# Kernel optimization log

Hardware: AMD Instinct MI355X
Metric: run time of the kernel (lower is better)

The kernel has to match this reference:

```python
import jax, jax.numpy as jnp
import numpy as np

B, T, D, H = 4, 2048, 1024, 16
DH = D // H  # 64

def setup_inputs() -> dict:
    key = jax.random.key(0)
    ks = jax.random.split(key, 5)
    scale = 1.0 / np.sqrt(DH)
    return {
        "x": jax.random.normal(ks[0], (B, T, D), dtype=jnp.float32),
        "Wq": jax.random.normal(ks[1], (H, DH, DH), dtype=jnp.float32) * scale,
        "Wk": jax.random.normal(ks[2], (H, DH, DH), dtype=jnp.float32) * scale,
        "Wv": jax.random.normal(ks[3], (H, DH, DH), dtype=jnp.float32) * scale,
        "Wout": jax.random.normal(ks[4], (D, D), dtype=jnp.float32) * (1.0 / np.sqrt(D)),
    }

def reference(x, Wq, Wk, Wv, Wout):
    b, t, d = x.shape
    xh = x.reshape(b, t, H, DH)  # split into heads (b, t, h, dh)
    # torch Linear: y = x @ W.T -> contract input dim with last dim of W
    Q = jnp.einsum('bthd,hed->bthe', xh, Wq)
    K = jnp.einsum('bthd,hed->bthe', xh, Wk)
    V = jnp.einsum('bthd,hed->bthe', xh, Wv)
    scale = 1.0 / jnp.sqrt(jnp.asarray(DH, dtype=x.dtype))
    scores = jnp.einsum('bqhd,bkhd->bhqk', Q, K) * scale  # (b, h, T, T)
    weights = jax.nn.softmax(scores, axis=-1)
    attn = jnp.einsum('bhqk,bkhd->bqhd', weights, V)  # (b, T, h, dh)
    attn = attn.reshape(b, t, d)  # concat heads
    return attn @ Wout.T
```

## Files before the change

### kernel.cpp

```cpp
#include <hip/hip_runtime.h>
#include <hip/hip_bf16.h>

#define BB 4
#define TT 2048
#define DD 1024
#define HH 16

typedef __bf16 bf16;
typedef __bf16 bf16x8 __attribute__((ext_vector_type(8)));
typedef __bf16 bf16x4 __attribute__((ext_vector_type(4)));
typedef float f32x4 __attribute__((ext_vector_type(4)));
typedef float f32x16 __attribute__((ext_vector_type(16)));
typedef unsigned int u32;
typedef u32 u32x4 __attribute__((ext_vector_type(4)));

#define MFMA16(a, b, c) __builtin_amdgcn_mfma_f32_16x16x32_bf16(a, b, c, 0, 0, 0)
#define MFMA32(a, b, c) __builtin_amdgcn_mfma_f32_32x32x16_bf16(a, b, c, 0, 0, 0)

#define C1 0.18033688011112042f

typedef __attribute__((address_space(1))) const u32 gau32;
typedef __attribute__((address_space(3))) u32 lau32;
static __device__ __forceinline__ void gload_lds16(const void* g, void* l) {
    __builtin_amdgcn_global_load_lds((gau32*)g, (lau32*)l, 16, 0, 0);
}

static __device__ __forceinline__ u32 cvtpk(float a, float b) {
    u32 r;
    asm("v_cvt_pk_bf16_f32 %0, %1, %2" : "=v"(r) : "v"(a), "v"(b));
    return r;
}

static __device__ __forceinline__ float rexp2(float x) {
#if __has_builtin(__builtin_amdgcn_exp2f)
    return __builtin_amdgcn_exp2f(x);
#else
    float r;
    asm("v_exp_f32 %0, %1" : "=v"(r) : "v"(x));
    return r;
#endif
}

__global__ __launch_bounds__(256) void k_cvtall(const float* __restrict__ wo, const float* __restrict__ wq,
                                                const float* __restrict__ wk, const float* __restrict__ wv,
                                                bf16* __restrict__ ob, bf16* __restrict__ qb,
                                                bf16* __restrict__ kb, bf16* __restrict__ vb) {
    int i = (blockIdx.x * 256 + threadIdx.x) * 4;
    const float* s;
    bf16* d;
    int off;
    if (i < DD * DD) {
        s = wo; d = ob; off = i;
    } else {
        int j = i - DD * DD;
        int wsel = j >> 16;
        off = j & 65535;
        s = wsel == 0 ? wq : (wsel == 1 ? wk : wv);
        d = wsel == 0 ? qb : (wsel == 1 ? kb : vb);
    }
    f32x4 v = *reinterpret_cast<const f32x4*>(s + off);
    bf16x4 r;
    r[0] = (bf16)v[0]; r[1] = (bf16)v[1]; r[2] = (bf16)v[2]; r[3] = (bf16)v[3];
    *reinterpret_cast<bf16x4*>(d + off) = r;
}

__global__ __launch_bounds__(256) void k_qkv(const float* __restrict__ x,
                                             const bf16* __restrict__ Wq,
                                             const bf16* __restrict__ Wk,
                                             const bf16* __restrict__ Wv,
                                             bf16* __restrict__ Qb,
                                             bf16* __restrict__ Kb,
                                             bf16* __restrict__ VT) {
    __shared__ float xs[4][32 * 64];
    const int w = threadIdx.x >> 6, lane = threadIdx.x & 63;
    const int c = lane & 15, g = lane >> 4;
    const int bh = blockIdx.y;
    const int b = bh >> 4, h = bh & 15;
    const int tb = blockIdx.x * 128 + w * 32;

    float* xw = xs[w];
    {
        const int lr = lane >> 4;
        const int lch = lane & 15;
#pragma unroll
        for (int p = 0; p < 8; p++) {
            const int r = p * 4 + lr;
            const int ch = lch ^ (r & 15);
            gload_lds16(x + ((size_t)(b * TT + tb + r)) * DD + h * 64 + ch * 4,
                        (char*)xw + p * 1024);
        }
    }
    asm volatile("s_waitcnt vmcnt(0)" ::: "memory");

    bf16x8 a[2][2];
#pragma unroll
    for (int s = 0; s < 2; s++)
#pragma unroll
        for (int dt = 0; dt < 2; dt++) {
            const int r = 16 * s + c;
            const int c0 = 8 * dt + 2 * g;
            f32x4 lo = *reinterpret_cast<const f32x4*>(&xw[r * 64 + (c0 ^ (r & 15)) * 4]);
            f32x4 hi = *reinterpret_cast<const f32x4*>(&xw[r * 64 + ((c0 + 1) ^ (r & 15)) * 4]);
            u32x4 u;
            u[0] = cvtpk(lo[0], lo[1]);
            u[1] = cvtpk(lo[2], lo[3]);
            u[2] = cvtpk(hi[0], hi[1]);
            u[3] = cvtpk(hi[2], hi[3]);
            a[s][dt] = __builtin_bit_cast(bf16x8, u);
        }

    const bf16* const Ws[3] = {Wq, Wk, Wv};
    f32x4 acc[3][2][4];
#pragma unroll
    for (int m = 0; m < 3; m++)
#pragma unroll
        for (int s = 0; s < 2; s++)
#pragma unroll
            for (int e = 0; e < 4; e++)
#pragma unroll
                for (int r = 0; r < 4; r++) acc[m][s][e][r] = 0.0f;

#pragma unroll
    for (int m = 0; m < 3; m++) {
#pragma unroll
        for (int eg = 0; eg < 4; eg++) {
#pragma unroll
            for (int dt = 0; dt < 2; dt++) {
                bf16x8 bf = *reinterpret_cast<const bf16x8*>(
                    Ws[m] + (size_t)(h * 64 + 16 * eg + c) * 64 + 32 * dt + 8 * g);
#pragma unroll
                for (int s = 0; s < 2; s++)
                    acc[m][s][eg] = MFMA16(a[s][dt], bf, acc[m][s][eg]);
            }
        }
    }

    bf16* const outs[2] = {Qb, Kb};
#pragma unroll
    for (int m = 0; m < 2; m++)
#pragma unroll
        for (int s = 0; s < 2; s++)
#pragma unroll
            for (int eg = 0; eg < 4; eg++)
#pragma unroll
                for (int r = 0; r < 4; r++) {
                    int t = tb + 16 * s + 4 * g + r;
                    float sv = acc[m][s][eg][r];
                    if (m == 0) sv *= C1;
                    outs[m][((size_t)bh * TT + t) * 64 + 16 * eg + c] = (bf16)sv;
                }

    bf16* vl = (bf16*)xs[w];
#pragma unroll
    for (int s = 0; s < 2; s++)
#pragma unroll
        for (int eg = 0; eg < 4; eg++) {
            bf16x4 v4;
#pragma unroll
            for (int r = 0; r < 4; r++) v4[r] = (bf16)acc[2][s][eg][r];
            *reinterpret_cast<bf16x4*>(&vl[(16 * eg + c) * 40 + 16 * s + 4 * g]) = v4;
        }
#pragma unroll
    for (int n = 0; n < 8; n++) {
        const int np = (n & 4) | ((n & 1) << 1) | ((n >> 1) & 1);
        bf16x4 v = *reinterpret_cast<bf16x4*>(&vl[lane * 40 + 4 * n]);
        *reinterpret_cast<bf16x4*>(&VT[((size_t)bh * 64 + lane) * TT + tb + 4 * np]) = v;
    }
}

#define ATTN_TILE(SKC, SVC, SKN, SVN, T)                                                        \
    do {                                                                                        \
        if ((T) < 31) {                                                                         \
            gload_lds16(kgsrc0 + (size_t)((T) + 1) * 4096, &(SKN)[w * 512]);                    \
            gload_lds16(kgsrc1 + (size_t)((T) + 1) * 4096, &(SKN)[2048 + w * 512]);             \
            gload_lds16(vgsrc0 + (size_t)((T) + 1) * 64, &(SVN)[w * 512]);                      \
            gload_lds16(vgsrc1 + (size_t)((T) + 1) * 64, &(SVN)[2048 + w * 512]);               \
        }                                                                                       \
        f32x16 s0, s1;                                                                          \
        _Pragma("unroll") for (int i = 0; i < 16; i++) { s0[i] = 0.0f; s1[i] = 0.0f; }          \
        __builtin_amdgcn_s_setprio(1);                                                          \
        _Pragma("unroll") for (int d = 0; d < 4; d++) {                                         \
            bf16x8 ka0 = *reinterpret_cast<const bf16x8*>(&(SKC)[roff + d * 1024 + goff0]);     \
            bf16x8 ka1 = *reinterpret_cast<const bf16x8*>(&(SKC)[roff + d * 1024 + goff1]);     \
            s0 = MFMA32(ka0, aq[d], s0);                                                        \
            s1 = MFMA32(ka1, aq[d], s1);                                                        \
        }                                                                                       \
        __builtin_amdgcn_s_setprio(0);                                                          \
        u32 pk[2][4][2];                                                                        \
        _Pragma("unroll") for (int r = 0; r < 16; r++) { float p = rexp2(s0[r]); psum += p; s0[r] = p; } \
        _Pragma("unroll") for (int r = 0; r < 16; r++) { float p = rexp2(s1[r]); psum += p; s1[r] = p; } \
        _Pragma("unroll") for (int m = 0; m < 4; m++)                                           \
            _Pragma("unroll") for (int b2 = 0; b2 < 2; b2++) {                                  \
                pk[0][m][b2] = cvtpk(s0[4 * m + 2 * b2], s0[4 * m + 2 * b2 + 1]);               \
                pk[1][m][b2] = cvtpk(s1[4 * m + 2 * b2], s1[4 * m + 2 * b2 + 1]);               \
            }                                                                                   \
        __builtin_amdgcn_s_setprio(1);                                                          \
        _Pragma("unroll") for (int kt = 0; kt < 4; kt++) {                                      \
            u32x4 pu;                                                                           \
            pu[0] = pk[kt >> 1][2 * (kt & 1)][0];                                               \
            pu[1] = pk[kt >> 1][2 * (kt & 1)][1];                                               \
            pu[2] = pk[kt >> 1][2 * (kt & 1) + 1][0];                                           \
            pu[3] = pk[kt >> 1][2 * (kt & 1) + 1][1];                                           \
            bf16x8 pb = __builtin_bit_cast(bf16x8, pu);                                         \
            bf16x8 va0 = *reinterpret_cast<const bf16x8*>(&(SVC)[roff + kt * 1024 + goff0]);    \
            bf16x8 va1 = *reinterpret_cast<const bf16x8*>(&(SVC)[roff + kt * 1024 + goff1]);    \
            o0 = MFMA32(va0, pb, o0);                                                           \
            o1 = MFMA32(va1, pb, o1);                                                           \
        }                                                                                       \
        __builtin_amdgcn_s_setprio(0);                                                         \
        __syncthreads();                                                                        \
    } while (0)

__global__ __launch_bounds__(256, 4) void k_attn(const bf16* __restrict__ Qb,
                                                 const bf16* __restrict__ Kb,
                                                 const bf16* __restrict__ VT,
                                                 bf16* __restrict__ AO) {
    __shared__ bf16 sK[2][64 * 64];
    __shared__ bf16 sV[2][64 * 64];
    const int w = threadIdx.x >> 6, lane = threadIdx.x & 63;
    const int q = lane & 31, h = lane >> 5;
    const int bid = blockIdx.x;
    const int swz = (bid & 7) * 128 + (bid >> 3);
    const int bh = swz >> 4;
    const int qb = (swz & 15) * 128 + w * 32;
    const bf16* Qh = Qb + (size_t)bh * TT * 64;
    const bf16* Kh = Kb + (size_t)bh * TT * 64;
    const bf16* Vh = VT + (size_t)bh * 64 * TT;

    const int gp = lane & 7;
    int st[2], sj[2];
#pragma unroll
    for (int p = 0; p < 2; p++) {
        const int rp = p * 32 + w * 8 + (lane >> 3);
        const int u_ = rp & 15, J1 = rp >> 4;
        const int e_ = gp ^ (u_ & 7);
        st[p] = 32 * (e_ >> 2) + 16 * (e_ & 1) + u_;
        sj[p] = 2 * J1 + ((e_ >> 1) & 1);
    }
    const bf16* kgsrc0 = Kh + (size_t)st[0] * 64 + sj[0] * 8;
    const bf16* kgsrc1 = Kh + (size_t)st[1] * 64 + sj[1] * 8;
    const bf16* vgsrc0 = Vh + (size_t)st[0] * TT + sj[0] * 8;
    const bf16* vgsrc1 = Vh + (size_t)st[1] * TT + sj[1] * 8;

    gload_lds16(kgsrc0, &sK[0][w * 512]);
    gload_lds16(kgsrc1, &sK[0][2048 + w * 512]);
    gload_lds16(vgsrc0, &sV[0][w * 512]);
    gload_lds16(vgsrc1, &sV[0][2048 + w * 512]);

    bf16x8 aq[4];
#pragma unroll
    for (int d = 0; d < 4; d++)
        aq[d] = *reinterpret_cast<const bf16x8*>(Qh + (size_t)(qb + q) * 64 + 16 * d + 8 * h);

    const int vv = 2 * h + ((q >> 4) & 1);
    const int gl = vv ^ (q & 3);
    const int gb2 = (q >> 2) & 1;
    const int roff = (q & 15) * 64;
    const int goff0 = (4 * gb2 + gl) * 8;
    const int goff1 = (4 * (1 ^ gb2) + gl) * 8;

    f32x16 o0, o1;
#pragma unroll
    for (int i = 0; i < 16; i++) { o0[i] = 0.0f; o1[i] = 0.0f; }
    float psum = 0.0f;

    __syncthreads();

    for (int tp = 0; tp < 16; tp++) {
        ATTN_TILE(sK[0], sV[0], sK[1], sV[1], 2 * tp);
        ATTN_TILE(sK[1], sV[1], sK[0], sV[0], 2 * tp + 1);
    }

    const float l = psum + __shfl_xor(psum, 32);
    const float linv = 1.0f / l;

    const size_t obase = ((size_t)bh * TT + qb + q) * 64;
#pragma unroll
    for (int dg = 0; dg < 2; dg++)
#pragma unroll
        for (int m = 0; m < 4; m++) {
            bf16x4 v;
#pragma unroll
            for (int j = 0; j < 4; j++) {
                const float ov = dg ? o1[4 * m + j] : o0[4 * m + j];
                v[j] = (bf16)(ov * linv);
            }
            *reinterpret_cast<bf16x4*>(AO + obase + 32 * dg + 8 * m + 4 * h) = v;
        }
}

#define OSTAGE(BUF, H)                                                                          \
    do {                                                                                        \
        const bf16* Ab = AO + ((size_t)(b * HH + (H)) * TT + t0) * 64;                          \
        const bf16* Bb = Wo + (size_t)nb * DD + (H) * 64;                                       \
        _Pragma("unroll") for (int p = 0; p < 4; p++) {                                         \
            const int r = p * 32 + w * 8 + (lane >> 3);                                         \
            const int jj = (lane & 7) ^ (r & 7);                                                \
            gload_lds16(Ab + (size_t)r * 64 + jj * 8, &sA[BUF][p * 2048 + w * 512]);            \
            gload_lds16(Bb + (size_t)r * DD + jj * 8, &sB[BUF][p * 2048 + w * 512]);            \
        }                                                                                       \
    } while (0)

__global__ __launch_bounds__(256, 2) void k_oproj(const bf16* __restrict__ AO,
                                                  const bf16* __restrict__ Wo,
                                                  float* __restrict__ out) {
    __shared__ bf16 sA[2][128 * 64];
    __shared__ bf16 sB[2][128 * 64];
    const int w = threadIdx.x >> 6, lane = threadIdx.x & 63;
    const int c = lane & 15, g = lane >> 4;
    const int bid = blockIdx.x;
    const int nb = (bid & 7) * 128;
    const int row0 = (bid >> 3) * 128;
    const int b = row0 >> 11;
    const int t0 = row0 & 2047;

    f32x4 acc[2][8];
#pragma unroll
    for (int s = 0; s < 2; s++)
#pragma unroll
        for (int ng = 0; ng < 8; ng++)
#pragma unroll
            for (int r = 0; r < 4; r++) acc[s][ng][r] = 0.0f;

    OSTAGE(0, 0);
    __syncthreads();

    int buf = 0;
#pragma unroll 1
    for (int hh = 0; hh < 16; hh++) {
        if (hh < 15) OSTAGE(buf ^ 1, hh + 1);
        const bf16* pa = sA[buf];
        const bf16* pb = sB[buf];
#pragma unroll
        for (int dt = 0; dt < 2; dt++) {
            const int gsw = ((4 * dt + g) ^ (c & 7)) * 8;
            bf16x8 aa[2];
#pragma unroll
            for (int s = 0; s < 2; s++)
                aa[s] = *reinterpret_cast<const bf16x8*>(&pa[(w * 32 + 16 * s + c) * 64 + gsw]);
            __builtin_amdgcn_s_setprio(1);
#pragma unroll
            for (int ng = 0; ng < 8; ng++) {
                bf16x8 bb = *reinterpret_cast<const bf16x8*>(&pb[(16 * ng + c) * 64 + gsw]);
#pragma unroll
                for (int s = 0; s < 2; s++)
                    acc[s][ng] = MFMA16(aa[s], bb, acc[s][ng]);
            }
            __builtin_amdgcn_s_setprio(0);
        }
        __syncthreads();
        buf ^= 1;
    }

    const int mb = row0 + w * 32;
#pragma unroll
    for (int s = 0; s < 2; s++)
#pragma unroll
        for (int ng = 0; ng < 8; ng++)
#pragma unroll
            for (int r = 0; r < 4; r++)
                out[(size_t)(mb + 16 * s + 4 * g + r) * DD + nb + 16 * ng + c] = acc[s][ng][r];
}

extern "C" void kernel_launch(void* const* d_in, const int* in_sizes, int n_in,
                              void* d_out, int out_size, void* d_ws, size_t ws_size,
                              hipStream_t stream) {
    const float* x = (const float*)d_in[0];
    const float* Wq = (const float*)d_in[1];
    const float* Wk = (const float*)d_in[2];
    const float* Wv = (const float*)d_in[3];
    const float* Wo = (const float*)d_in[4];
    float* out = (float*)d_out;

    char* ws = (char*)d_ws;
    bf16* Qb = (bf16*)(ws);
    bf16* Kb = (bf16*)(ws + (16ll << 20));
    bf16* VT = (bf16*)(ws + (32ll << 20));
    bf16* AO = (bf16*)(ws + (48ll << 20));
    bf16* Wob = (bf16*)(ws + (64ll << 20));
    bf16* Wqb = (bf16*)(ws + (66ll << 20));
    bf16* Wkb = (bf16*)(ws + (66ll << 20) + (128ll << 10));
    bf16* Wvb = (bf16*)(ws + (66ll << 20) + (256ll << 10));

    k_cvtall<<<1216, 256, 0, stream>>>(Wo, Wq, Wk, Wv, Wob, Wqb, Wkb, Wvb);
    k_qkv<<<dim3(TT / 128, BB * HH), 256, 0, stream>>>(x, Wqb, Wkb, Wvb, Qb, Kb, VT);
    k_attn<<<1024, 256, 0, stream>>>(Qb, Kb, VT, AO);
    k_oproj<<<512, 256, 0, stream>>>(AO, Wob, out);
}
```

Baseline: 140.1 us.

## Use 512-thread attention blocks with triple-buffered K/V LDS pipeline

```diff
diff --git a/kernel.cpp b/kernel.cpp
--- a/kernel.cpp
+++ b/kernel.cpp
@@ -168,13 +168,14 @@
     }
 }
 
-#define ATTN_TILE(SKC, SVC, SKN, SVN, T)                                                        \
+#define ATTN_STEP(SKC, SVC, SKP, SVP, T, ISSUE, VM)                                             \
     do {                                                                                        \
-        if ((T) < 31) {                                                                         \
-            gload_lds16(kgsrc0 + (size_t)((T) + 1) * 4096, &(SKN)[w * 512]);                    \
-            gload_lds16(kgsrc1 + (size_t)((T) + 1) * 4096, &(SKN)[2048 + w * 512]);             \
-            gload_lds16(vgsrc0 + (size_t)((T) + 1) * 64, &(SVN)[w * 512]);                      \
-            gload_lds16(vgsrc1 + (size_t)((T) + 1) * 64, &(SVN)[2048 + w * 512]);               \
+        asm volatile("s_waitcnt vmcnt(" VM ")" ::: "memory");                                   \
+        __builtin_amdgcn_s_barrier();                                                           \
+        __builtin_amdgcn_sched_barrier(0);                                                      \
+        if (ISSUE) {                                                                            \
+            gload_lds16(kgsrc + (size_t)((T) + 2) * 4096, &(SKP)[w * 512]);                     \
+            gload_lds16(vgsrc + (size_t)((T) + 2) * 64, &(SVP)[w * 512]);                       \
         }                                                                                       \
         f32x16 s0, s1;                                                                          \
         _Pragma("unroll") for (int i = 0; i < 16; i++) { s0[i] = 0.0f; s1[i] = 0.0f; }          \
@@ -208,44 +209,37 @@
             o1 = MFMA32(va1, pb, o1);                                                           \
         }                                                                                       \
         __builtin_amdgcn_s_setprio(0);                                                         \
-        __syncthreads();                                                                        \
     } while (0)
 
-__global__ __launch_bounds__(256, 4) void k_attn(const bf16* __restrict__ Qb,
+__global__ __launch_bounds__(512, 4) void k_attn(const bf16* __restrict__ Qb,
                                                  const bf16* __restrict__ Kb,
                                                  const bf16* __restrict__ VT,
                                                  bf16* __restrict__ AO) {
-    __shared__ bf16 sK[2][64 * 64];
-    __shared__ bf16 sV[2][64 * 64];
+    __shared__ bf16 sK[3][64 * 64];
+    __shared__ bf16 sV[3][64 * 64];
     const int w = threadIdx.x >> 6, lane = threadIdx.x & 63;
     const int q = lane & 31, h = lane >> 5;
     const int bid = blockIdx.x;
-    const int swz = (bid & 7) * 128 + (bid >> 3);
-    const int bh = swz >> 4;
-    const int qb = (swz & 15) * 128 + w * 32;
+    const int swz = (bid & 7) * 64 + (bid >> 3);
+    const int bh = swz >> 3;
+    const int qb = (swz & 7) * 256 + w * 32;
     const bf16* Qh = Qb + (size_t)bh * TT * 64;
     const bf16* Kh = Kb + (size_t)bh * TT * 64;
     const bf16* Vh = VT + (size_t)bh * 64 * TT;
 
     const int gp = lane & 7;
-    int st[2], sj[2];
-#pragma unroll
-    for (int p = 0; p < 2; p++) {
-        const int rp = p * 32 + w * 8 + (lane >> 3);
-        const int u_ = rp & 15, J1 = rp >> 4;
-        const int e_ = gp ^ (u_ & 7);
-        st[p] = 32 * (e_ >> 2) + 16 * (e_ & 1) + u_;
-        sj[p] = 2 * J1 + ((e_ >> 1) & 1);
-    }
-    const bf16* kgsrc0 = Kh + (size_t)st[0] * 64 + sj[0] * 8;
-    const bf16* kgsrc1 = Kh + (size_t)st[1] * 64 + sj[1] * 8;
-    const bf16* vgsrc0 = Vh + (size_t)st[0] * TT + sj[0] * 8;
-    const bf16* vgsrc1 = Vh + (size_t)st[1] * TT + sj[1] * 8;
-
-    gload_lds16(kgsrc0, &sK[0][w * 512]);
-    gload_lds16(kgsrc1, &sK[0][2048 + w * 512]);
-    gload_lds16(vgsrc0, &sV[0][w * 512]);
-    gload_lds16(vgsrc1, &sV[0][2048 + w * 512]);
+    const int rp = w * 8 + (lane >> 3);
+    const int u_ = rp & 15, J1 = rp >> 4;
+    const int e_ = gp ^ (u_ & 7);
+    const int st = 32 * (e_ >> 2) + 16 * (e_ & 1) + u_;
+    const int sj = 2 * J1 + ((e_ >> 1) & 1);
+    const bf16* kgsrc = Kh + (size_t)st * 64 + sj * 8;
+    const bf16* vgsrc = Vh + (size_t)st * TT + sj * 8;
+
+    gload_lds16(kgsrc, &sK[0][w * 512]);
+    gload_lds16(vgsrc, &sV[0][w * 512]);
+    gload_lds16(kgsrc + 4096, &sK[1][w * 512]);
+    gload_lds16(vgsrc + 64, &sV[1][w * 512]);
 
     bf16x8 aq[4];
 #pragma unroll
@@ -264,12 +258,15 @@
     for (int i = 0; i < 16; i++) { o0[i] = 0.0f; o1[i] = 0.0f; }
     float psum = 0.0f;
 
-    __syncthreads();
-
-    for (int tp = 0; tp < 16; tp++) {
-        ATTN_TILE(sK[0], sV[0], sK[1], sV[1], 2 * tp);
-        ATTN_TILE(sK[1], sV[1], sK[0], sV[0], 2 * tp + 1);
-    }
+#pragma unroll 1
+    for (int i = 0; i < 10; i++) {
+        const int t0 = 3 * i;
+        ATTN_STEP(sK[0], sV[0], sK[2], sV[2], t0, 1, "2");
+        ATTN_STEP(sK[1], sV[1], sK[0], sV[0], t0 + 1, 1, "2");
+        ATTN_STEP(sK[2], sV[2], sK[1], sV[1], t0 + 2, 1, "2");
+    }
+    ATTN_STEP(sK[0], sV[0], sK[2], sV[2], 30, 0, "2");
+    ATTN_STEP(sK[1], sV[1], sK[0], sV[0], 31, 0, "0");
 
     const float l = psum + __shfl_xor(psum, 32);
     const float linv = 1.0f / l;
@@ -384,6 +381,6 @@
 
     k_cvtall<<<1216, 256, 0, stream>>>(Wo, Wq, Wk, Wv, Wob, Wqb, Wkb, Wvb);
     k_qkv<<<dim3(TT / 128, BB * HH), 256, 0, stream>>>(x, Wqb, Wkb, Wvb, Qb, Kb, VT);
-    k_attn<<<1024, 256, 0, stream>>>(Qb, Kb, VT, AO);
+    k_attn<<<512, 512, 0, stream>>>(Qb, Kb, VT, AO);
     k_oproj<<<512, 256, 0, stream>>>(AO, Wob, out);
 }
```

Result: faster. 134.0 us, median of 3 (-4.3%).
